# Kernel tuning notes

Hardware: AMD Instinct MI355X
Metric: run time of the kernel (lower is better)

## Reference

```python
import jax, jax.numpy as jnp
import numpy as np

D_MODEL = 512
D_FFN = 1024
B, N = 8, 2048


def setup_inputs() -> dict:
    key = jax.random.key(0)
    k1, k2, k3, k4, k5, k6 = jax.random.split(key, 6)
    x = jax.random.normal(k1, (B, N, D_MODEL), dtype=jnp.float32)
    interaction_mask = jax.random.randint(k2, (B, N, N), 0, 2).astype(jnp.float32)
    s1 = 1.0 / np.sqrt(D_MODEL)
    s2 = 1.0 / np.sqrt(D_FFN)
    W1 = jax.random.uniform(k3, (D_MODEL, D_FFN), jnp.float32, -s1, s1)
    b1 = jax.random.uniform(k4, (D_FFN,), jnp.float32, -s1, s1)
    W2 = jax.random.uniform(k5, (D_FFN, 3 * D_MODEL), jnp.float32, -s2, s2)
    b2 = jax.random.uniform(k6, (3 * D_MODEL,), jnp.float32, -s2, s2)
    return {"x": x, "interaction_mask": interaction_mask,
            "W1": W1, "b1": b1, "W2": W2, "b2": b2}


def reference(x, interaction_mask, W1, b1, W2, b2):
    # 2-layer FFN: Linear -> ReLU -> Linear (identity)
    h = jax.nn.relu(x @ W1 + b1)           # [B, N, d_ffn]
    kqv = h @ W2 + b2                        # [B, N, 3*d_model]
    k, q, v = jnp.split(kqv, 3, axis=-1)     # each [B, N, d_model]
    scale = D_MODEL ** -0.5
    # softmax-free scaled dot-product
    attn = jnp.einsum("bqd,bkd->bqk", q, k) * scale  # [B, N, N]
    attn = attn * interaction_mask
    return jnp.einsum("bqk,bkd->bqd", attn, v)        # [B, N, d_model]
```

## Files before the change

kernel.cpp:

```cpp
#include <hip/hip_runtime.h>
#include <hip/hip_bf16.h>

typedef __attribute__((ext_vector_type(8))) short bf16x8;
typedef __attribute__((ext_vector_type(4))) float f32x4;

#define NB 8
#define NN 2048
#define DM 512
#define DF 1024

__device__ __forceinline__ ushort f2b(float f) {
  union { __hip_bfloat16 h; ushort u; } c;
  c.h = __float2bfloat16(f);
  return c.u;
}
__device__ __forceinline__ float b2f(ushort u) {
  union { ushort u; __hip_bfloat16 h; } c;
  c.u = u;
  return __bfloat162float(c.h);
}

typedef __attribute__((address_space(1))) const void gvoid_t;
typedef __attribute__((address_space(3))) void svoid_t;
__device__ __forceinline__ void gload16(const void* g, void* s) {
  __builtin_amdgcn_global_load_lds((gvoid_t*)g, (svoid_t*)s, 16, 0, 0);
}

__device__ __forceinline__ void gemm_core_128(
    const ushort* __restrict__ A, const ushort* __restrict__ B,
    int K, int brow, int bcol, f32x4 (&acc)[4][4], ushort* smem)
{
  const int tid = threadIdx.x;
  const int w = tid >> 6, l = tid & 63;
  const int sr = (w << 3) + (l >> 3);
  const int sc = (((l & 7) ^ (l >> 3)) << 3);
  const int fr = l & 15;
  const int arow = ((w >> 1) << 6) + fr;
  const int brw  = ((w & 1) << 6) + fr;
  char* base = (char*)smem;
  char* A0 = base;          char* B0 = base + 16384;
  char* A1 = base + 32768;  char* B1 = base + 49152;

#pragma unroll
  for (int m = 0; m < 4; m++)
#pragma unroll
    for (int n = 0; n < 4; n++)
      acc[m][n] = (f32x4){0.f, 0.f, 0.f, 0.f};

  const ushort* Ap = A + (long)(brow + sr) * K + sc;
  const ushort* Bp = B + (long)(bcol + sr) * K + sc;
  const int nkt = K >> 6;

  auto stage = [&](char* Ad, char* Bd, int kt) {
#pragma unroll
    for (int i = 0; i < 4; i++) {
      gload16(Ap + (long)i * 32 * K + kt * 64, Ad + i * 4096 + (w << 10));
      gload16(Bp + (long)i * 32 * K + kt * 64, Bd + i * 4096 + (w << 10));
    }
  };
  auto compute = [&](const char* As_, const char* Bs_) {
#pragma unroll
    for (int kk = 0; kk < 2; kk++) {
      const int cx = ((((kk << 2) + (l >> 4)) ^ (l & 7)) << 4);
      bf16x8 a[4], b[4];
#pragma unroll
      for (int m = 0; m < 4; m++)
        a[m] = *(const bf16x8*)(As_ + (arow + m * 16) * 128 + cx);
#pragma unroll
      for (int n = 0; n < 4; n++)
        b[n] = *(const bf16x8*)(Bs_ + (brw + n * 16) * 128 + cx);
#pragma unroll
      for (int m = 0; m < 4; m++)
#pragma unroll
        for (int n = 0; n < 4; n++)
          acc[m][n] = __builtin_amdgcn_mfma_f32_16x16x32_bf16(a[m], b[n], acc[m][n], 0, 0, 0);
    }
  };

  stage(A0, B0, 0);
  __syncthreads();
  for (int kt = 0; kt < nkt; kt += 2) {
    stage(A1, B1, kt + 1);
    compute(A0, B0);
    __syncthreads();
    if (kt + 2 < nkt) stage(A0, B0, kt + 2);
    compute(A1, B1);
    __syncthreads();
  }
}

__device__ __forceinline__ void gemm_core_128_sb(
    const ushort* __restrict__ A, const ushort* __restrict__ B,
    int K, int brow, int bcol, f32x4 (&acc)[4][4], ushort* smem)
{
  ushort* As = smem;
  ushort* Bs = smem + 128 * 64;
  const int tid = threadIdx.x;
  const int w = tid >> 6, l = tid & 63;
  const int sr = (w << 3) + (l >> 3);
  const int sc = (((l & 7) ^ (l >> 3)) << 3);
  char* AsB = (char*)As;
  char* BsB = (char*)Bs;
  const int fr = l & 15;
  const int arow = ((w >> 1) << 6) + fr;
  const int brw  = ((w & 1) << 6) + fr;

#pragma unroll
  for (int m = 0; m < 4; m++)
#pragma unroll
    for (int n = 0; n < 4; n++)
      acc[m][n] = (f32x4){0.f, 0.f, 0.f, 0.f};

  const ushort* Ap = A + (long)(brow + sr) * K + sc;
  const ushort* Bp = B + (long)(bcol + sr) * K + sc;
  const int nkt = K >> 6;
  for (int kt = 0; kt < nkt; ++kt) {
#pragma unroll
    for (int i = 0; i < 4; i++) {
      gload16(Ap + (long)i * 32 * K, AsB + i * 4096 + (w << 10));
      gload16(Bp + (long)i * 32 * K, BsB + i * 4096 + (w << 10));
    }
    Ap += 64; Bp += 64;
    __syncthreads();
#pragma unroll
    for (int kk = 0; kk < 2; kk++) {
      const int cx = ((((kk << 2) + (l >> 4)) ^ (l & 7)) << 4);
      bf16x8 a[4], b[4];
#pragma unroll
      for (int m = 0; m < 4; m++)
        a[m] = *(const bf16x8*)(AsB + (arow + m * 16) * 128 + cx);
#pragma unroll
      for (int n = 0; n < 4; n++)
        b[n] = *(const bf16x8*)(BsB + (brw + n * 16) * 128 + cx);
#pragma unroll
      for (int m = 0; m < 4; m++)
#pragma unroll
        for (int n = 0; n < 4; n++)
          acc[m][n] = __builtin_amdgcn_mfma_f32_16x16x32_bf16(a[m], b[n], acc[m][n], 0, 0, 0);
    }
    __syncthreads();
  }
}

__device__ __forceinline__ void acc_to_lds_bf16(f32x4 (&acc)[4][4], ushort* smem) {
  const int tid = threadIdx.x, w = tid >> 6, l = tid & 63;
  const int r0l = ((w >> 1) << 6) + ((l >> 4) << 2);
  const int c0l = ((w & 1) << 6) + (l & 15);
#pragma unroll
  for (int n = 0; n < 4; n++)
#pragma unroll
    for (int m = 0; m < 4; m++)
#pragma unroll
      for (int j = 0; j < 4; j++)
        smem[(r0l + m * 16 + j) * 128 + (c0l + n * 16)] = f2b(acc[m][n][j]);
}


__global__ __launch_bounds__(256) void k_cvt(const float* __restrict__ in,
                                             ushort* __restrict__ out) {
  const long i = ((long)blockIdx.x * 256 + threadIdx.x) << 2;
  const float4 v = *(const float4*)(in + i);
  ushort4 o;
  o.x = f2b(v.x); o.y = f2b(v.y); o.z = f2b(v.z); o.w = f2b(v.w);
  *(ushort4*)(out + i) = o;
}

__global__ __launch_bounds__(256) void k_trw(const float* __restrict__ in, ushort* __restrict__ out,
                                             int R, int C) {
  __shared__ float t[32][33];
  const int c0 = blockIdx.x << 5, r0 = blockIdx.y << 5;
  const int tx = threadIdx.x & 31, ty = threadIdx.x >> 5;
#pragma unroll
  for (int j = 0; j < 32; j += 8)
    t[ty + j][tx] = in[(long)(r0 + ty + j) * C + (c0 + tx)];
  __syncthreads();
#pragma unroll
  for (int j = 0; j < 32; j += 8)
    out[(long)(c0 + ty + j) * R + (r0 + tx)] = f2b(t[tx][ty + j]);
}

__global__ __launch_bounds__(256) void k_gemm1(const ushort* __restrict__ xb,
                                               const ushort* __restrict__ w1t,
                                               const float* __restrict__ b1,
                                               ushort* __restrict__ hb) {
  __shared__ ushort smem[128 * 256];
  f32x4 acc[4][4];
  const int brow = blockIdx.x << 7, bcol = blockIdx.y << 7;
  gemm_core_128(xb, w1t, DM, brow, bcol, acc, smem);
  const int tid = threadIdx.x, w = tid >> 6, l = tid & 63;
  const int c0l = ((w & 1) << 6) + (l & 15);
#pragma unroll
  for (int n = 0; n < 4; n++) {
    const float bias = b1[bcol + c0l + n * 16];
#pragma unroll
    for (int m = 0; m < 4; m++)
#pragma unroll
      for (int j = 0; j < 4; j++) {
        float v = acc[m][n][j] + bias;
        acc[m][n][j] = v > 0.f ? v : 0.f;
      }
  }
  acc_to_lds_bf16(acc, smem);
  __syncthreads();
  const int rb = tid >> 4, cb = tid & 15;
#pragma unroll
  for (int i = 0; i < 8; i++) {
    const int row = i * 16 + rb;
    bf16x8 s = *(const bf16x8*)(smem + row * 128 + cb * 8);
    *(bf16x8*)(hb + (long)(brow + row) * DF + bcol + cb * 8) = s;
  }
}

__global__ __launch_bounds__(256) void k_gemm2(const ushort* __restrict__ hb,
                                               const ushort* __restrict__ w2t,
                                               const float* __restrict__ b2,
                                               ushort* __restrict__ kb,
                                               ushort* __restrict__ qb,
                                               ushort* __restrict__ vtb) {
  __shared__ ushort smem[128 * 256];
  f32x4 acc[4][4];
  const int brow = blockIdx.x << 7, bcol = blockIdx.y << 7;
  gemm_core_128(hb, w2t, DF, brow, bcol, acc, smem);
  const int seg = bcol >> 9;
  const float sc = (seg == 1) ? 0.04419417382415922f : 1.0f;
  const int tid = threadIdx.x, w = tid >> 6, l = tid & 63;
  const int c0l = ((w & 1) << 6) + (l & 15);
#pragma unroll
  for (int n = 0; n < 4; n++) {
    const float bias = b2[bcol + c0l + n * 16];
#pragma unroll
    for (int m = 0; m < 4; m++)
#pragma unroll
      for (int j = 0; j < 4; j++)
        acc[m][n][j] = (acc[m][n][j] + bias) * sc;
  }
  acc_to_lds_bf16(acc, smem);
  __syncthreads();
  const int clb = bcol - (seg << 9);
  if (seg < 2) {
    ushort* dst = (seg == 0) ? kb : qb;
    const int rb = tid >> 4, cb = tid & 15;
#pragma unroll
    for (int i = 0; i < 8; i++) {
      const int row = i * 16 + rb;
      bf16x8 s = *(const bf16x8*)(smem + row * 128 + cb * 8);
      *(bf16x8*)(dst + (long)(brow + row) * DM + clb + cb * 8) = s;
    }
  } else {
    const int batch = brow >> 11;
    const int rbase = brow & 2047;
    const int c = tid & 127, rc = tid >> 7;
    ushort* vt = vtb + (long)batch * DM * NN + (long)(clb + c) * NN + rbase;
#pragma unroll
    for (int it = 0; it < 8; ++it) {
      const int chunk = rc * 8 + it;
      bf16x8 o;
#pragma unroll
      for (int j = 0; j < 8; ++j)
        o[j] = (short)smem[(chunk * 8 + j) * 128 + c];
      *(bf16x8*)(vt + chunk * 8) = o;
    }
  }
}

__global__ __launch_bounds__(256) void k_qk(const ushort* __restrict__ qb,
                                            const ushort* __restrict__ kb,
                                            const float* __restrict__ mask,
                                            ushort* __restrict__ Sbuf) {
  __shared__ ushort smem[128 * 128];
  const int orig = blockIdx.x;
  const int batch = orig & 7;
  const int t = orig >> 3;
  const int bx = t & 15, by = t >> 4;
  const int brow = bx << 7, bcol = by << 7;
  const ushort* A = qb + (long)batch * NN * DM;
  const ushort* Bm = kb + (long)batch * NN * DM;
  const float* mk = mask + (long)batch * NN * NN;
  ushort* S = Sbuf + (long)batch * NN * NN;
  f32x4 acc[4][4];
  gemm_core_128_sb(A, Bm, DM, brow, bcol, acc, smem);
  acc_to_lds_bf16(acc, smem);
  __syncthreads();
  const int tid = threadIdx.x, rb = tid >> 4, cb = tid & 15;
#pragma unroll
  for (int i = 0; i < 8; i++) {
    const int row = i * 16 + rb;
    const long goff = (long)(brow + row) * NN + bcol + cb * 8;
    bf16x8 s = *(const bf16x8*)(smem + row * 128 + cb * 8);
    const f32x4 m0 = __builtin_nontemporal_load((const f32x4*)(mk + goff));
    const f32x4 m1 = __builtin_nontemporal_load((const f32x4*)(mk + goff + 4));
    bf16x8 o;
    o[0] = (short)f2b(b2f((ushort)s[0]) * m0[0]);
    o[1] = (short)f2b(b2f((ushort)s[1]) * m0[1]);
    o[2] = (short)f2b(b2f((ushort)s[2]) * m0[2]);
    o[3] = (short)f2b(b2f((ushort)s[3]) * m0[3]);
    o[4] = (short)f2b(b2f((ushort)s[4]) * m1[0]);
    o[5] = (short)f2b(b2f((ushort)s[5]) * m1[1]);
    o[6] = (short)f2b(b2f((ushort)s[6]) * m1[2]);
    o[7] = (short)f2b(b2f((ushort)s[7]) * m1[3]);
    *(bf16x8*)(S + goff) = o;
  }
}

__global__ __launch_bounds__(256) void k_pv(const ushort* __restrict__ Sbuf,
                                            const ushort* __restrict__ vtb,
                                            float* __restrict__ out) {
  __shared__ ushort smem[128 * 256];
  const int batch = blockIdx.z;
  const ushort* A = Sbuf + (long)batch * NN * NN;
  const ushort* Bm = vtb + (long)batch * DM * NN;
  float* op = out + (long)batch * NN * DM;
  f32x4 acc[4][4];
  const int brow = blockIdx.x << 7, bcol = blockIdx.y << 7;
  gemm_core_128(A, Bm, NN, brow, bcol, acc, smem);
  float* fs = (float*)smem;
  const int tid = threadIdx.x, w = tid >> 6, l = tid & 63;
  const int r0l = ((w >> 1) << 6) + ((l >> 4) << 2);
  const int c0l = ((w & 1) << 6) + (l & 15);
#pragma unroll
  for (int n = 0; n < 4; n++)
#pragma unroll
    for (int m = 0; m < 4; m++)
#pragma unroll
      for (int j = 0; j < 4; j++)
        fs[(r0l + m * 16 + j) * 128 + (c0l + n * 16)] = acc[m][n][j];
  __syncthreads();
  const int rg = tid >> 5, l32 = tid & 31;
#pragma unroll
  for (int p = 0; p < 16; ++p) {
    const int row = p * 8 + rg;
    const float4 v = *(const float4*)(fs + row * 128 + l32 * 4);
    *(float4*)(op + (long)(brow + row) * DM + bcol + l32 * 4) = v;
  }
}

extern "C" void kernel_launch(void* const* d_in, const int* in_sizes, int n_in,
                              void* d_out, int out_size, void* d_ws, size_t ws_size,
                              hipStream_t stream) {
  const float* x    = (const float*)d_in[0];
  const float* mask = (const float*)d_in[1];
  const float* W1   = (const float*)d_in[2];
  const float* b1   = (const float*)d_in[3];
  const float* W2   = (const float*)d_in[4];
  const float* b2   = (const float*)d_in[5];
  float* out = (float*)d_out;

  char* ws = (char*)d_ws;
  size_t off = 0;
  auto alloc = [&](size_t n) { char* p = ws + off; off += (n + 255) & ~(size_t)255; return p; };
  ushort* xb  = (ushort*)alloc((size_t)NB * NN * DM * 2);
  ushort* hb  = (ushort*)alloc((size_t)NB * NN * DF * 2);
  ushort* w1t = (ushort*)alloc((size_t)DF * DM * 2);
  ushort* w2t = (ushort*)alloc((size_t)3 * DM * DF * 2);
  ushort* kb  = (ushort*)alloc((size_t)NB * NN * DM * 2);
  ushort* qb  = (ushort*)alloc((size_t)NB * NN * DM * 2);
  ushort* vtb = (ushort*)alloc((size_t)NB * NN * DM * 2);
  ushort* Sbuf = (ushort*)alloc((size_t)NB * NN * NN * 2);

  k_cvt<<<dim3(8192), dim3(256), 0, stream>>>(x, xb);
  k_trw<<<dim3(DF / 32, DM / 32), dim3(256), 0, stream>>>(W1, w1t, DM, DF);
  k_trw<<<dim3(3 * DM / 32, DF / 32), dim3(256), 0, stream>>>(W2, w2t, DF, 3 * DM);
  k_gemm1<<<dim3(NB * NN / 128, DF / 128), dim3(256), 0, stream>>>(xb, w1t, b1, hb);
  k_gemm2<<<dim3(NB * NN / 128, 3 * DM / 128), dim3(256), 0, stream>>>(hb, w2t, b2, kb, qb, vtb);
  k_qk<<<dim3(2048), dim3(256), 0, stream>>>(qb, kb, mask, Sbuf);
  k_pv<<<dim3(NN / 128, DM / 128, NB), dim3(256), 0, stream>>>(Sbuf, vtb, out);
}
```

Measured before the change: 210.1 us.

## Enlarge QK tile to 256x128 with 512 threads and interleave PV batches

```diff
diff --git a/kernel.cpp b/kernel.cpp
--- a/kernel.cpp
+++ b/kernel.cpp
@@ -89,59 +89,6 @@
   }
 }
 
-__device__ __forceinline__ void gemm_core_128_sb(
-    const ushort* __restrict__ A, const ushort* __restrict__ B,
-    int K, int brow, int bcol, f32x4 (&acc)[4][4], ushort* smem)
-{
-  ushort* As = smem;
-  ushort* Bs = smem + 128 * 64;
-  const int tid = threadIdx.x;
-  const int w = tid >> 6, l = tid & 63;
-  const int sr = (w << 3) + (l >> 3);
-  const int sc = (((l & 7) ^ (l >> 3)) << 3);
-  char* AsB = (char*)As;
-  char* BsB = (char*)Bs;
-  const int fr = l & 15;
-  const int arow = ((w >> 1) << 6) + fr;
-  const int brw  = ((w & 1) << 6) + fr;
-
-#pragma unroll
-  for (int m = 0; m < 4; m++)
-#pragma unroll
-    for (int n = 0; n < 4; n++)
-      acc[m][n] = (f32x4){0.f, 0.f, 0.f, 0.f};
-
-  const ushort* Ap = A + (long)(brow + sr) * K + sc;
-  const ushort* Bp = B + (long)(bcol + sr) * K + sc;
-  const int nkt = K >> 6;
-  for (int kt = 0; kt < nkt; ++kt) {
-#pragma unroll
-    for (int i = 0; i < 4; i++) {
-      gload16(Ap + (long)i * 32 * K, AsB + i * 4096 + (w << 10));
-      gload16(Bp + (long)i * 32 * K, BsB + i * 4096 + (w << 10));
-    }
-    Ap += 64; Bp += 64;
-    __syncthreads();
-#pragma unroll
-    for (int kk = 0; kk < 2; kk++) {
-      const int cx = ((((kk << 2) + (l >> 4)) ^ (l & 7)) << 4);
-      bf16x8 a[4], b[4];
-#pragma unroll
-      for (int m = 0; m < 4; m++)
-        a[m] = *(const bf16x8*)(AsB + (arow + m * 16) * 128 + cx);
-#pragma unroll
-      for (int n = 0; n < 4; n++)
-        b[n] = *(const bf16x8*)(BsB + (brw + n * 16) * 128 + cx);
-#pragma unroll
-      for (int m = 0; m < 4; m++)
-#pragma unroll
-        for (int n = 0; n < 4; n++)
-          acc[m][n] = __builtin_amdgcn_mfma_f32_16x16x32_bf16(a[m], b[n], acc[m][n], 0, 0, 0);
-    }
-    __syncthreads();
-  }
-}
-
 __device__ __forceinline__ void acc_to_lds_bf16(f32x4 (&acc)[4][4], ushort* smem) {
   const int tid = threadIdx.x, w = tid >> 6, l = tid & 63;
   const int r0l = ((w >> 1) << 6) + ((l >> 4) << 2);
@@ -263,42 +210,101 @@
   }
 }
 
-__global__ __launch_bounds__(256) void k_qk(const ushort* __restrict__ qb,
+__global__ __launch_bounds__(512) void k_qk(const ushort* __restrict__ qb,
                                             const ushort* __restrict__ kb,
                                             const float* __restrict__ mask,
                                             ushort* __restrict__ Sbuf) {
-  __shared__ ushort smem[128 * 128];
-  const int orig = blockIdx.x;
-  const int batch = orig & 7;
-  const int t = orig >> 3;
-  const int bx = t & 15, by = t >> 4;
-  const int brow = bx << 7, bcol = by << 7;
+  __shared__ ushort smem[24576];
+  const int bid = blockIdx.x;
+  const int batch = bid & 7;
+  const int t = bid >> 3;
+  const int brow = (t & 7) << 8;
+  const int bcol = (t >> 3) << 7;
   const ushort* A = qb + (long)batch * NN * DM;
-  const ushort* Bm = kb + (long)batch * NN * DM;
+  const ushort* B = kb + (long)batch * NN * DM;
   const float* mk = mask + (long)batch * NN * NN;
   ushort* S = Sbuf + (long)batch * NN * NN;
+
+  const int tid = threadIdx.x;
+  const int w = tid >> 6, l = tid & 63;
+  const int wr = w & 3, wc = w >> 2;
+  const int fr = l & 15;
+  char* AsB = (char*)smem;
+  char* BsB = AsB + 32768;
+
   f32x4 acc[4][4];
-  gemm_core_128_sb(A, Bm, DM, brow, bcol, acc, smem);
-  acc_to_lds_bf16(acc, smem);
-  __syncthreads();
-  const int tid = threadIdx.x, rb = tid >> 4, cb = tid & 15;
-#pragma unroll
-  for (int i = 0; i < 8; i++) {
-    const int row = i * 16 + rb;
-    const long goff = (long)(brow + row) * NN + bcol + cb * 8;
-    bf16x8 s = *(const bf16x8*)(smem + row * 128 + cb * 8);
-    const f32x4 m0 = __builtin_nontemporal_load((const f32x4*)(mk + goff));
-    const f32x4 m1 = __builtin_nontemporal_load((const f32x4*)(mk + goff + 4));
-    bf16x8 o;
-    o[0] = (short)f2b(b2f((ushort)s[0]) * m0[0]);
-    o[1] = (short)f2b(b2f((ushort)s[1]) * m0[1]);
-    o[2] = (short)f2b(b2f((ushort)s[2]) * m0[2]);
-    o[3] = (short)f2b(b2f((ushort)s[3]) * m0[3]);
-    o[4] = (short)f2b(b2f((ushort)s[4]) * m1[0]);
-    o[5] = (short)f2b(b2f((ushort)s[5]) * m1[1]);
-    o[6] = (short)f2b(b2f((ushort)s[6]) * m1[2]);
-    o[7] = (short)f2b(b2f((ushort)s[7]) * m1[3]);
-    *(bf16x8*)(S + goff) = o;
+#pragma unroll
+  for (int m = 0; m < 4; m++)
+#pragma unroll
+    for (int n = 0; n < 4; n++)
+      acc[m][n] = (f32x4){0.f, 0.f, 0.f, 0.f};
+
+  const int srow = (w << 3) + (l >> 3);
+  const int sc = (((l & 7) ^ (l >> 3)) << 3);
+  const ushort* Ap = A + (long)(brow + srow) * DM + sc;
+  const ushort* Bp = B + (long)(bcol + srow) * DM + sc;
+
+  for (int kt = 0; kt < 8; ++kt) {
+#pragma unroll
+    for (int i = 0; i < 4; i++)
+      gload16(Ap + (long)i * 64 * DM + kt * 64, AsB + i * 8192 + (w << 10));
+#pragma unroll
+    for (int i = 0; i < 2; i++)
+      gload16(Bp + (long)i * 64 * DM + kt * 64, BsB + i * 8192 + (w << 10));
+    __syncthreads();
+#pragma unroll
+    for (int kk = 0; kk < 2; kk++) {
+      const int cx = ((((kk << 2) + (l >> 4)) ^ (l & 7)) << 4);
+      bf16x8 b[4], a[4];
+#pragma unroll
+      for (int n = 0; n < 4; n++)
+        b[n] = *(const bf16x8*)(BsB + ((wc << 6) + (n << 4) + fr) * 128 + cx);
+#pragma unroll
+      for (int m = 0; m < 4; m++)
+        a[m] = *(const bf16x8*)(AsB + ((wr << 6) + (m << 4) + fr) * 128 + cx);
+#pragma unroll
+      for (int m = 0; m < 4; m++)
+#pragma unroll
+        for (int n = 0; n < 4; n++)
+          acc[m][n] = __builtin_amdgcn_mfma_f32_16x16x32_bf16(a[m], b[n], acc[m][n], 0, 0, 0);
+    }
+    __syncthreads();
+  }
+
+  const int rb = tid >> 4, cb = tid & 15;
+#pragma unroll
+  for (int h = 0; h < 2; ++h) {
+    if ((wr >> 1) == h) {
+      const int r0l = ((wr & 1) << 6) + ((l >> 4) << 2);
+      const int c0l = (wc << 6) + fr;
+#pragma unroll
+      for (int n = 0; n < 4; n++)
+#pragma unroll
+        for (int m = 0; m < 4; m++)
+#pragma unroll
+          for (int j = 0; j < 4; j++)
+            smem[(r0l + m * 16 + j) * 128 + (c0l + n * 16)] = f2b(acc[m][n][j]);
+    }
+    __syncthreads();
+#pragma unroll
+    for (int i = 0; i < 4; i++) {
+      const int row = i * 32 + rb;
+      const long goff = (long)(brow + h * 128 + row) * NN + bcol + cb * 8;
+      bf16x8 s = *(const bf16x8*)(smem + row * 128 + cb * 8);
+      const f32x4 m0 = __builtin_nontemporal_load((const f32x4*)(mk + goff));
+      const f32x4 m1 = __builtin_nontemporal_load((const f32x4*)(mk + goff + 4));
+      bf16x8 o;
+      o[0] = (short)f2b(b2f((ushort)s[0]) * m0[0]);
+      o[1] = (short)f2b(b2f((ushort)s[1]) * m0[1]);
+      o[2] = (short)f2b(b2f((ushort)s[2]) * m0[2]);
+      o[3] = (short)f2b(b2f((ushort)s[3]) * m0[3]);
+      o[4] = (short)f2b(b2f((ushort)s[4]) * m1[0]);
+      o[5] = (short)f2b(b2f((ushort)s[5]) * m1[1]);
+      o[6] = (short)f2b(b2f((ushort)s[6]) * m1[2]);
+      o[7] = (short)f2b(b2f((ushort)s[7]) * m1[3]);
+      *(bf16x8*)(S + goff) = o;
+    }
+    __syncthreads();
   }
 }
 
@@ -306,12 +312,15 @@
                                             const ushort* __restrict__ vtb,
                                             float* __restrict__ out) {
   __shared__ ushort smem[128 * 256];
-  const int batch = blockIdx.z;
+  const int bid = blockIdx.x;
+  const int batch = bid & 7;
+  const int t = bid >> 3;
+  const int brow = (t & 15) << 7;
+  const int bcol = (t >> 4) << 7;
   const ushort* A = Sbuf + (long)batch * NN * NN;
   const ushort* Bm = vtb + (long)batch * DM * NN;
   float* op = out + (long)batch * NN * DM;
   f32x4 acc[4][4];
-  const int brow = blockIdx.x << 7, bcol = blockIdx.y << 7;
   gemm_core_128(A, Bm, NN, brow, bcol, acc, smem);
   float* fs = (float*)smem;
   const int tid = threadIdx.x, w = tid >> 6, l = tid & 63;
@@ -362,6 +371,6 @@
   k_trw<<<dim3(3 * DM / 32, DF / 32), dim3(256), 0, stream>>>(W2, w2t, DF, 3 * DM);
   k_gemm1<<<dim3(NB * NN / 128, DF / 128), dim3(256), 0, stream>>>(xb, w1t, b1, hb);
   k_gemm2<<<dim3(NB * NN / 128, 3 * DM / 128), dim3(256), 0, stream>>>(hb, w2t, b2, kb, qb, vtb);
-  k_qk<<<dim3(2048), dim3(256), 0, stream>>>(qb, kb, mask, Sbuf);
-  k_pv<<<dim3(NN / 128, DM / 128, NB), dim3(256), 0, stream>>>(Sbuf, vtb, out);
-}
+  k_qk<<<dim3(1024), dim3(512), 0, stream>>>(qb, kb, mask, Sbuf);
+  k_pv<<<dim3(512), dim3(256), 0, stream>>>(Sbuf, vtb, out);
+}
```

Result: no change. 211.9 us (+0.9%).
